# Optimization experiments

Measured on AMD Instinct MI355X. Metric: run time of the kernel, lower is better.

## Reference

```python
import jax, jax.numpy as jnp
import numpy as np

VOCAB = 32000
NUM_STATE = 256
NLABEL = 64
BATCH = 128
MAXLEN = 256
# transition init scale chosen so E[e^2]*S*a^2/3 ~= 1 -> per-step magnitude ~constant
TRANS_A = 0.208


def setup_inputs() -> dict:
    key = jax.random.key(0)
    k1, k2, k3, k4 = jax.random.split(key, 4)
    sentences = jax.random.randint(k1, (BATCH, MAXLEN), 0, VOCAB, dtype=jnp.int64)
    # original init: input.weight ~ U(0.5, 0.5) (constant 0.5). Use U(0.25, 0.75) so the
    # emission stays bounded away from 0 (it is divided by) while not being degenerate.
    emb = jax.random.uniform(k2, (VOCAB, NUM_STATE), minval=0.25, maxval=0.75, dtype=jnp.float32)
    transition = jax.random.uniform(k3, (NUM_STATE, NUM_STATE), minval=-TRANS_A, maxval=TRANS_A, dtype=jnp.float32)
    output = jax.random.uniform(k4, (NUM_STATE, NLABEL), minval=-0.5, maxval=0.5, dtype=jnp.float32)
    return {"sentences": sentences, "emb": emb, "transition": transition, "output": output}


def reference(sentences, emb, transition, output):
    # emission: [maxlen, batch, num_state]
    em = emb[sentences.T]

    def step_fwd(carry, e):  # carry: [B,S]
        nxt = jnp.einsum('ij,bj->bi', transition, carry) * e
        return nxt, nxt

    _, fw_rest = jax.lax.scan(step_fwd, em[0], em[1:])
    forwards = jnp.concatenate([em[:1], fw_rest], axis=0)  # [L,B,S]

    em_rev = em[::-1]

    def step_bwd(carry, e):  # uses transition^T
        nxt = jnp.einsum('ji,bj->bi', transition, carry) * e
        return nxt, nxt

    _, bw_rest = jax.lax.scan(step_bwd, em_rev[0], em_rev[1:])
    backwards = jnp.concatenate([em_rev[:1], bw_rest], axis=0)[::-1]  # time-aligned [L,B,S]

    expected_count = forwards * backwards / em
    score = jnp.einsum('lbs,sn->lbn', expected_count, output)
    return score.transpose(1, 0, 2)  # [batch, maxlen, nlabel]
```

## Files before the change

### kernel.cpp

```cpp
#include <hip/hip_runtime.h>
#include <hip/hip_bf16.h>


typedef _Float16 half8 __attribute__((ext_vector_type(8)));
typedef _Float16 half4 __attribute__((ext_vector_type(4)));
typedef float    f32x4 __attribute__((ext_vector_type(4)));
typedef unsigned long long u64;

#define LL 256
#define BB 128
#define SS 256
#define BT 16
#define RSTR8 67
#define RSTRO 65

static __device__ __forceinline__ f32x4 mfma16f(half8 a, half8 b, f32x4 c) {
  return __builtin_amdgcn_mfma_f32_16x16x32_f16(a, b, c, 0, 0, 0);
}

static __device__ __forceinline__ void lds_barrier() {
  __asm__ __volatile__("s_waitcnt lgkmcnt(0)\n\ts_barrier" ::: "memory");
}

static __device__ __forceinline__ u64 pack4(f32x4 v) {
  union { half4 h; u64 u; } x;
  x.h[0] = (_Float16)v[0];
  x.h[1] = (_Float16)v[1];
  x.h[2] = (_Float16)v[2];
  x.h[3] = (_Float16)v[3];
  return x.u;
}

static __device__ __forceinline__ half8 read_frag_s(const u64* plane, int row,
                                                    int kt, int q, int stride8) {
  const int o = row * stride8 + kt * 8 + q * 2;
  union { u64 u[2]; half8 v; } x;
  x.u[0] = plane[o];
  x.u[1] = plane[o + 1];
  return x.v;
}

__global__ __launch_bounds__(1024, 4)
void hmm_chain(const int* __restrict__ sent, const float* __restrict__ emb,
               const float* __restrict__ T, _Float16* __restrict__ fwh,
               _Float16* __restrict__ gh)
{
  __shared__ u64 s_carry[2][BT * RSTR8];
  __shared__ int s_tok[BT * 257];

  const int tid  = threadIdx.x;
  const int lane = tid & 63;
  const int w    = tid >> 6;
  const int m    = lane & 15;
  const int q    = lane >> 4;

  const int  bid = blockIdx.x;
  const bool fwd = (bid < 8);
  const int  bg0 = (fwd ? bid : bid - 8) * BT;
  _Float16* const obuf = fwd ? fwh : gh;
  const int  st  = 16 * w + 4 * q;

  for (int idx = tid; idx < BT * LL; idx += 1024) {
    int bb = idx >> 8, l2 = idx & 255;
    s_tok[bb * 257 + l2] = sent[(bg0 + bb) * LL + l2];
  }
  __syncthreads();

  half8 a_hi[8];
#pragma unroll
  for (int kt = 0; kt < 8; ++kt) {
    const int r0 = 16 * w + m;
    const int kb = 32 * kt + 8 * q;
    float v[8];
    if (fwd) {
      f32x4 f0 = *(const f32x4*)(T + r0 * 256 + kb);
      f32x4 f1 = *(const f32x4*)(T + r0 * 256 + kb + 4);
#pragma unroll
      for (int j = 0; j < 4; ++j) { v[j] = f0[j]; v[4 + j] = f1[j]; }
    } else {
#pragma unroll
      for (int j = 0; j < 8; ++j) v[j] = T[(kb + j) * 256 + r0];
    }
    half8 hi;
#pragma unroll
    for (int j = 0; j < 8; ++j) hi[j] = (_Float16)v[j];
    a_hi[kt] = hi;
  }

  const int l0 = fwd ? 0 : (LL - 1);
  {
    const int tok0 = s_tok[m * 257 + l0];
    f32x4 e0 = *(const f32x4*)(emb + (size_t)tok0 * 256 + st);
    u64 pc = pack4(e0);
    f32x4 one = 1.0f;
    u64 po = fwd ? pc : pack4(one);
    *(u64*)(obuf + (size_t)(l0 * BB + bg0 + m) * SS + st) = po;
    s_carry[0][m * RSTR8 + 4 * w + q] = pc;
  }

  f32x4 em_pref;
  {
    const int l1 = fwd ? 1 : (LL - 2);
    const int tok1 = s_tok[m * 257 + l1];
    em_pref = *(const f32x4*)(emb + (size_t)tok1 * 256 + st);
  }
  __syncthreads();

  for (int s = 1; s < LL; ++s) {
    const int l  = fwd ? s : (LL - 1) - s;
    const int rb = (s - 1) & 1, wb = s & 1;

    const u64* pr = &s_carry[rb][0];
    half8 bfr[8];
#pragma unroll
    for (int kt = 0; kt < 8; ++kt)
      bfr[kt] = read_frag_s(pr, m, kt, q, RSTR8);

    f32x4 em_now = em_pref;
    {
      const int ln = fwd ? (s + 1 < LL ? s + 1 : LL - 1)
                         : ((LL - 2) - s > 0 ? (LL - 2) - s : 0);
      const int tokn = s_tok[m * 257 + ln];
      em_pref = *(const f32x4*)(emb + (size_t)tokn * 256 + st);
    }

    f32x4 hh = 0.0f;
#pragma unroll
    for (int kt = 0; kt < 8; ++kt)
      hh = mfma16f(a_hi[kt], bfr[kt], hh);
    f32x4 v  = hh;
    f32x4 cn = v * em_now;

    u64 p0 = pack4(cn);
    s_carry[wb][m * RSTR8 + 4 * w + q] = p0;
    u64 sv = fwd ? p0 : pack4(v);
    *(u64*)(obuf + (size_t)(l * BB + bg0 + m) * SS + st) = sv;
    lds_barrier();
  }
}

__global__ __launch_bounds__(256, 2)
void hmm_score(const _Float16* __restrict__ fwh, const _Float16* __restrict__ gh,
               const float* __restrict__ outm, float* __restrict__ score)
{
  __shared__ u64 p_pl[64 * RSTR8];
  __shared__ u64 o_pl[64 * RSTRO];

  const int tid  = threadIdx.x;
  const int lane = tid & 63;
  const int w    = tid >> 6;
  const int rh   = w >> 1;
  const int np   = w & 1;
  const int m    = lane & 15;
  const int q    = lane >> 4;
  const int R0   = blockIdx.x * 64;

  {
    _Float16* o_h = (_Float16*)o_pl;
    for (int i = tid; i < 4096; i += 256) {
      f32x4 v = *(const f32x4*)(outm + i * 4);
      int k = i >> 4, n0 = (i & 15) * 4;
#pragma unroll
      for (int r = 0; r < 4; ++r)
        o_h[(n0 + r) * (RSTRO * 4) + k] = (_Float16)v[r];
    }
  }

  for (int idx = tid; idx < 64 * 64; idx += 256) {
    int row = idx >> 6, c = idx & 63;
    union { u64 u; half4 h; } a, b, p;
    a.u = *(const u64*)(fwh + (size_t)(R0 + row) * 256 + c * 4);
    b.u = *(const u64*)(gh  + (size_t)(R0 + row) * 256 + c * 4);
    p.h = a.h * b.h;
    p_pl[row * RSTR8 + c] = p.u;
  }
  lds_barrier();

  f32x4 acc[2][2];
#pragma unroll
  for (int j = 0; j < 2; ++j)
#pragma unroll
    for (int jn = 0; jn < 2; ++jn) acc[j][jn] = 0.0f;

#pragma unroll
  for (int kt = 0; kt < 8; ++kt) {
    half8 of[2];
#pragma unroll
    for (int jn = 0; jn < 2; ++jn)
      of[jn] = read_frag_s(o_pl, 16 * (2 * np + jn) + m, kt, q, RSTRO);
#pragma unroll
    for (int j = 0; j < 2; ++j) {
      half8 pf = read_frag_s(p_pl, 32 * rh + 16 * j + m, kt, q, RSTR8);
#pragma unroll
      for (int jn = 0; jn < 2; ++jn)
        acc[j][jn] = mfma16f(pf, of[jn], acc[j][jn]);
    }
  }

#pragma unroll
  for (int j = 0; j < 2; ++j) {
#pragma unroll
    for (int jn = 0; jn < 2; ++jn) {
#pragma unroll
      for (int r = 0; r < 4; ++r) {
        int row = R0 + 32 * rh + 16 * j + 4 * q + r;
        int l = row >> 7, b = row & 127;
        score[(size_t)b * 16384 + l * 64 + 16 * (2 * np + jn) + m] = acc[j][jn][r];
      }
    }
  }
}

extern "C" void kernel_launch(void* const* d_in, const int* in_sizes, int n_in,
                              void* d_out, int out_size, void* d_ws, size_t ws_size,
                              hipStream_t stream) {
  (void)in_sizes; (void)n_in; (void)out_size; (void)ws_size;
  const int*   sent = (const int*)d_in[0];
  const float* emb  = (const float*)d_in[1];
  const float* T    = (const float*)d_in[2];
  const float* outm = (const float*)d_in[3];
  _Float16* fwh = (_Float16*)d_ws;
  _Float16* gh  = fwh + (size_t)LL * BB * SS;

  hmm_chain<<<16, 1024, 0, stream>>>(sent, emb, T, fwh, gh);
  hmm_score<<<512, 256, 0, stream>>>(fwh, gh, outm, (float*)d_out);
}
```

Before: 293.8 us.

## Halve chain block to 512 threads with two M-tiles per wave

The recurrence kernel now runs 8 waves per block instead of 16. Each wave computes two 16-row state tiles and reuses the same B fragments read from LDS for both MFMA chains. This is meant to cut the per-step barrier cost and the redundant LDS fragment reads, and to give each wave two independent MFMA chains to interleave. The cost is double the register use for A fragments and more serial work per wave on each step.

```diff
diff --git a/kernel.cpp b/kernel.cpp
--- a/kernel.cpp
+++ b/kernel.cpp
@@ -40,7 +40,7 @@
   return x.v;
 }
 
-__global__ __launch_bounds__(1024, 4)
+__global__ __launch_bounds__(512, 2)
 void hmm_chain(const int* __restrict__ sent, const float* __restrict__ emb,
                const float* __restrict__ T, _Float16* __restrict__ fwh,
                _Float16* __restrict__ gh)
@@ -58,51 +58,59 @@
   const bool fwd = (bid < 8);
   const int  bg0 = (fwd ? bid : bid - 8) * BT;
   _Float16* const obuf = fwd ? fwh : gh;
-  const int  st  = 16 * w + 4 * q;
-
-  for (int idx = tid; idx < BT * LL; idx += 1024) {
+
+  for (int idx = tid; idx < BT * LL; idx += 512) {
     int bb = idx >> 8, l2 = idx & 255;
     s_tok[bb * 257 + l2] = sent[(bg0 + bb) * LL + l2];
   }
   __syncthreads();
 
-  half8 a_hi[8];
-#pragma unroll
-  for (int kt = 0; kt < 8; ++kt) {
-    const int r0 = 16 * w + m;
-    const int kb = 32 * kt + 8 * q;
-    float v[8];
-    if (fwd) {
-      f32x4 f0 = *(const f32x4*)(T + r0 * 256 + kb);
-      f32x4 f1 = *(const f32x4*)(T + r0 * 256 + kb + 4);
-#pragma unroll
-      for (int j = 0; j < 4; ++j) { v[j] = f0[j]; v[4 + j] = f1[j]; }
-    } else {
-#pragma unroll
-      for (int j = 0; j < 8; ++j) v[j] = T[(kb + j) * 256 + r0];
-    }
-    half8 hi;
-#pragma unroll
-    for (int j = 0; j < 8; ++j) hi[j] = (_Float16)v[j];
-    a_hi[kt] = hi;
+  half8 a_h[2][8];
+#pragma unroll
+  for (int mt = 0; mt < 2; ++mt) {
+#pragma unroll
+    for (int kt = 0; kt < 8; ++kt) {
+      const int r0 = 32 * w + 16 * mt + m;
+      const int kb = 32 * kt + 8 * q;
+      float v[8];
+      if (fwd) {
+        f32x4 f0 = *(const f32x4*)(T + r0 * 256 + kb);
+        f32x4 f1 = *(const f32x4*)(T + r0 * 256 + kb + 4);
+#pragma unroll
+        for (int j = 0; j < 4; ++j) { v[j] = f0[j]; v[4 + j] = f1[j]; }
+      } else {
+#pragma unroll
+        for (int j = 0; j < 8; ++j) v[j] = T[(kb + j) * 256 + r0];
+      }
+      half8 hi;
+#pragma unroll
+      for (int j = 0; j < 8; ++j) hi[j] = (_Float16)v[j];
+      a_h[mt][kt] = hi;
+    }
   }
 
   const int l0 = fwd ? 0 : (LL - 1);
   {
     const int tok0 = s_tok[m * 257 + l0];
-    f32x4 e0 = *(const f32x4*)(emb + (size_t)tok0 * 256 + st);
-    u64 pc = pack4(e0);
-    f32x4 one = 1.0f;
-    u64 po = fwd ? pc : pack4(one);
-    *(u64*)(obuf + (size_t)(l0 * BB + bg0 + m) * SS + st) = po;
-    s_carry[0][m * RSTR8 + 4 * w + q] = pc;
-  }
-
-  f32x4 em_pref;
+#pragma unroll
+    for (int mt = 0; mt < 2; ++mt) {
+      const int st = 32 * w + 16 * mt + 4 * q;
+      f32x4 e0 = *(const f32x4*)(emb + (size_t)tok0 * 256 + st);
+      u64 pc = pack4(e0);
+      f32x4 one = 1.0f;
+      u64 po = fwd ? pc : pack4(one);
+      *(u64*)(obuf + (size_t)(l0 * BB + bg0 + m) * SS + st) = po;
+      s_carry[0][m * RSTR8 + 8 * w + 4 * mt + q] = pc;
+    }
+  }
+
+  f32x4 em_pref[2];
   {
     const int l1 = fwd ? 1 : (LL - 2);
     const int tok1 = s_tok[m * 257 + l1];
-    em_pref = *(const f32x4*)(emb + (size_t)tok1 * 256 + st);
+#pragma unroll
+    for (int mt = 0; mt < 2; ++mt)
+      em_pref[mt] = *(const f32x4*)(emb + (size_t)tok1 * 256 + 32 * w + 16 * mt + 4 * q);
   }
   __syncthreads();
 
@@ -116,25 +124,35 @@
     for (int kt = 0; kt < 8; ++kt)
       bfr[kt] = read_frag_s(pr, m, kt, q, RSTR8);
 
-    f32x4 em_now = em_pref;
+    f32x4 em_now[2];
+#pragma unroll
+    for (int mt = 0; mt < 2; ++mt) em_now[mt] = em_pref[mt];
     {
       const int ln = fwd ? (s + 1 < LL ? s + 1 : LL - 1)
                          : ((LL - 2) - s > 0 ? (LL - 2) - s : 0);
       const int tokn = s_tok[m * 257 + ln];
-      em_pref = *(const f32x4*)(emb + (size_t)tokn * 256 + st);
-    }
-
-    f32x4 hh = 0.0f;
-#pragma unroll
-    for (int kt = 0; kt < 8; ++kt)
-      hh = mfma16f(a_hi[kt], bfr[kt], hh);
-    f32x4 v  = hh;
-    f32x4 cn = v * em_now;
-
-    u64 p0 = pack4(cn);
-    s_carry[wb][m * RSTR8 + 4 * w + q] = p0;
-    u64 sv = fwd ? p0 : pack4(v);
-    *(u64*)(obuf + (size_t)(l * BB + bg0 + m) * SS + st) = sv;
+#pragma unroll
+      for (int mt = 0; mt < 2; ++mt)
+        em_pref[mt] = *(const f32x4*)(emb + (size_t)tokn * 256 + 32 * w + 16 * mt + 4 * q);
+    }
+
+    f32x4 hh0 = 0.0f, hh1 = 0.0f;
+#pragma unroll
+    for (int kt = 0; kt < 8; ++kt) {
+      hh0 = mfma16f(a_h[0][kt], bfr[kt], hh0);
+      hh1 = mfma16f(a_h[1][kt], bfr[kt], hh1);
+    }
+    f32x4 v[2] = { hh0, hh1 };
+
+#pragma unroll
+    for (int mt = 0; mt < 2; ++mt) {
+      const int st = 32 * w + 16 * mt + 4 * q;
+      f32x4 cn = v[mt] * em_now[mt];
+      u64 p0 = pack4(cn);
+      s_carry[wb][m * RSTR8 + 8 * w + 4 * mt + q] = p0;
+      u64 sv = fwd ? p0 : pack4(v[mt]);
+      *(u64*)(obuf + (size_t)(l * BB + bg0 + m) * SS + st) = sv;
+    }
     lds_barrier();
   }
 }
@@ -222,6 +240,6 @@
   _Float16* fwh = (_Float16*)d_ws;
   _Float16* gh  = fwh + (size_t)LL * BB * SS;
 
-  hmm_chain<<<16, 1024, 0, stream>>>(sent, emb, T, fwh, gh);
+  hmm_chain<<<16, 512, 0, stream>>>(sent, emb, T, fwh, gh);
   hmm_score<<<512, 256, 0, stream>>>(fwh, gh, outm, (float*)d_out);
 }
```

After: 302.3 us. +2.9%, slower.
